# Kernel tuning notes

Measured on AMD Instinct MI355X. Metric: run time of the kernel, lower is better.

The kernel has to match this reference:

```python
import jax, jax.numpy as jnp
import numpy as np

N_HEADS = 16
HEAD_DIM = 64
HIDDEN = 1024


def setup_inputs() -> dict:
    key = jax.random.key(0)
    kx, kq, kk, kv, ko = jax.random.split(key, 5)
    B, S = 1, 4096
    # xavier_uniform for Linear(hidden, n_heads*head_dim): limit = sqrt(6/(fan_in+fan_out))
    lim = float(np.sqrt(6.0 / (HIDDEN + N_HEADS * HEAD_DIM)))
    x = jax.random.normal(kx, (B, S, HIDDEN), dtype=jnp.float32)
    wq = jax.random.uniform(kq, (N_HEADS * HEAD_DIM, HIDDEN), jnp.float32, -lim, lim)
    wk = jax.random.uniform(kk, (N_HEADS * HEAD_DIM, HIDDEN), jnp.float32, -lim, lim)
    wv = jax.random.uniform(kv, (N_HEADS * HEAD_DIM, HIDDEN), jnp.float32, -lim, lim)
    wo = jax.random.uniform(ko, (HIDDEN, N_HEADS * HEAD_DIM), jnp.float32, -lim, lim)
    return {"x": x, "wq": wq, "wk": wk, "wv": wv, "wo": wo}


def reference(x, wq, wk, wv, wo):
    B, S, _ = x.shape
    scale = HEAD_DIM ** -0.5
    # project and split heads: [B, H, S, D]
    def proj(w):
        return jnp.einsum('bsh,eh->bse', x, w).reshape(B, S, N_HEADS, HEAD_DIM).transpose(0, 2, 1, 3)
    q, k, v = proj(wq), proj(wk), proj(wv)
    scores = jnp.einsum('bhqd,bhkd->bhqk', q, k) * scale  # [B,H,S,S]
    causal = jnp.tril(jnp.ones((S, S), dtype=bool))
    scores = jnp.where(causal, scores, -jnp.inf)
    probs = jax.nn.softmax(scores, axis=-1)
    out = jnp.einsum('bhqk,bhkd->bhqd', probs, v)  # [B,H,S,D]
    out = out.transpose(0, 2, 1, 3).reshape(B, S, N_HEADS * HEAD_DIM)
    return jnp.einsum('bse,he->bsh', out, wo)
```

## Files before the change

### kernel.cpp

```cpp
#include <hip/hip_runtime.h>
#include <hip/hip_bf16.h>
#include <stdint.h>

typedef unsigned short u16;
typedef float f32x4 __attribute__((ext_vector_type(4)));
typedef __bf16 bf16x8 __attribute__((ext_vector_type(8)));
typedef u16 u16x8 __attribute__((ext_vector_type(8)));

#define GL2LDS16(g, l)                                                          \
  __builtin_amdgcn_global_load_lds(                                             \
      (const __attribute__((address_space(1))) unsigned int*)(g),               \
      (__attribute__((address_space(3))) unsigned int*)(l), 16, 0, 0)

#if __has_builtin(__builtin_amdgcn_exp2f)
#define EXP2(x) __builtin_amdgcn_exp2f(x)
#else
#define EXP2(x) exp2f(x)
#endif

#define SOFTMAX_SC 0.18033688f

__device__ __forceinline__ u16 f2bf(float f) {
  uint32_t u = __builtin_bit_cast(uint32_t, f);
  return (u16)((u + 0x7FFFu + ((u >> 16) & 1u)) >> 16);
}

__device__ __forceinline__ float bf2f(u16 b) {
  return __builtin_bit_cast(float, (uint32_t)b << 16);
}

__device__ __forceinline__ uint32_t cvt_pk_bf16(float lo, float hi) {
  uint32_t r;
  asm("v_cvt_pk_bf16_f32 %0, %1, %2" : "=v"(r) : "v"(lo), "v"(hi));
  return r;
}

__device__ __forceinline__ void cast8(const float* __restrict__ s,
                                      u16* __restrict__ d) {
  const float4* p = (const float4*)s;
  float4 a = p[0], b = p[1];
  uint4 o;
  o.x = cvt_pk_bf16(a.x, a.y);
  o.y = cvt_pk_bf16(a.z, a.w);
  o.z = cvt_pk_bf16(b.x, b.y);
  o.w = cvt_pk_bf16(b.z, b.w);
  *(uint4*)d = o;
}

__global__ __launch_bounds__(256) void cast_kernel(const float* __restrict__ s,
                                                   u16* __restrict__ d, int n) {
  int i = (blockIdx.x * 256 + threadIdx.x) * 8;
  if (i >= n) return;
  cast8(s + i, d + i);
}

__global__ __launch_bounds__(256) void cast4_kernel(const float* __restrict__ s0,
                                                    const float* __restrict__ s1,
                                                    const float* __restrict__ s2,
                                                    const float* __restrict__ s3,
                                                    u16* __restrict__ d) {
  int b = blockIdx.x >> 9;
  int i = ((blockIdx.x & 511) * 256 + threadIdx.x) * 8;
  const float* s = (b == 0) ? s0 : (b == 1) ? s1 : (b == 2) ? s2 : s3;
  cast8(s + i, d + ((size_t)b << 20) + i);
}

template <int MB>
__device__ __forceinline__ void mfma16(f32x4 (&acc)[8][4], const bf16x8 (&af)[4],
                                       const bf16x8 (&bfr)[4]) {
  asm volatile("s_waitcnt lgkmcnt(0)" ::: "memory");
  __builtin_amdgcn_sched_barrier(0);
  __builtin_amdgcn_s_setprio(1);
#pragma unroll
  for (int j = 0; j < 4; ++j)
#pragma unroll
    for (int n = 0; n < 4; ++n)
      acc[MB + j][n] = __builtin_amdgcn_mfma_f32_16x16x32_bf16(
          af[j], bfr[n], acc[MB + j][n], 0, 0, 0);
  __builtin_amdgcn_s_setprio(0);
}

__global__ __launch_bounds__(512, 2) void gemm8k(const u16* __restrict__ A,
                                                 const u16* __restrict__ B,
                                                 u16* __restrict__ C, int M,
                                                 int N, int K, int scaleq) {
  __shared__ u16 As[4][128 * 64];
  __shared__ u16 Bs[4][128 * 64];
  const int tid = threadIdx.x;
  const int lane = tid & 63;
  const int l15 = lane & 15, lhi = lane >> 4;
  const int wave = tid >> 6;
  const int wm = wave >> 2, wn = wave & 3;
  int bid = blockIdx.y * gridDim.x + blockIdx.x;
  const int cpx = (gridDim.x * gridDim.y) >> 3;
  bid = (bid & 7) * cpx + (bid >> 3);
  const int m0 = (bid / gridDim.x) * 256, n0 = (bid % gridDim.x) * 256;
  const int nt = K >> 6;

  int aoff[2][8], boff[2][4];
#pragma unroll
  for (int ks = 0; ks < 2; ++ks) {
    const int sl = ((ks * 4 + lhi) ^ (l15 & 7)) << 4;
#pragma unroll
    for (int m = 0; m < 8; ++m) aoff[ks][m] = (m * 16 + l15) * 128 + sl;
#pragma unroll
    for (int n = 0; n < 4; ++n)
      boff[ks][n] = ((wn & 1) * 64 + n * 16 + l15) * 128 + sl;
  }

  auto stA = [&](int T, int h) {
    u16* lb = As[(T & 1) * 2 + h];
#pragma unroll
    for (int i = 0; i < 2; ++i) {
      int c = tid + i * 512;
      int row = c >> 3;
      int scol = ((c & 7) ^ (row & 7)) * 8;
      GL2LDS16(A + (size_t)(m0 + h * 128 + row) * K + T * 64 + scol,
               (char*)lb + c * 16);
    }
  };
  auto stB = [&](int T, int h) {
    u16* lb = Bs[(T & 1) * 2 + h];
#pragma unroll
    for (int i = 0; i < 2; ++i) {
      int c = tid + i * 512;
      int row = c >> 3;
      int scol = ((c & 7) ^ (row & 7)) * 8;
      GL2LDS16(B + (size_t)(n0 + h * 128 + row) * K + T * 64 + scol,
               (char*)lb + c * 16);
    }
  };

  f32x4 acc[8][4] = {};

  stA(0, 0); stA(0, 1); stB(0, 0); stB(0, 1);
  asm volatile("s_waitcnt vmcnt(0)" ::: "memory");
  __builtin_amdgcn_s_barrier();

  for (int i = 0; i < nt / 2; ++i) {
    const int e = 2 * i, o = e + 1;
    const char* Ae = (const char*)As[wm];
    const char* Be = (const char*)Bs[wn >> 1];
    const char* Ao = (const char*)As[2 + wm];
    const char* Bo = (const char*)Bs[2 + (wn >> 1)];
    bf16x8 af[4], bfr[4];
    const bool pre = (e + 2) < nt;

    stA(o, 0); stA(o, 1);
    asm volatile("s_waitcnt vmcnt(4)" ::: "memory");
    __builtin_amdgcn_s_barrier();
#pragma unroll
    for (int j = 0; j < 4; ++j) af[j] = *(const bf16x8*)(Ae + aoff[0][j]);
#pragma unroll
    for (int n = 0; n < 4; ++n) bfr[n] = *(const bf16x8*)(Be + boff[0][n]);
    mfma16<0>(acc, af, bfr);
    __builtin_amdgcn_s_barrier();
#pragma unroll
    for (int j = 0; j < 4; ++j) af[j] = *(const bf16x8*)(Ae + aoff[0][4 + j]);
    stB(o, 0); stB(o, 1);
    __builtin_amdgcn_s_barrier();
    mfma16<4>(acc, af, bfr);
    __builtin_amdgcn_s_barrier();
#pragma unroll
    for (int j = 0; j < 4; ++j) af[j] = *(const bf16x8*)(Ae + aoff[1][j]);
#pragma unroll
    for (int n = 0; n < 4; ++n) bfr[n] = *(const bf16x8*)(Be + boff[1][n]);
    __builtin_amdgcn_s_barrier();
    mfma16<0>(acc, af, bfr);
    __builtin_amdgcn_s_barrier();
#pragma unroll
    for (int j = 0; j < 4; ++j) af[j] = *(const bf16x8*)(Ae + aoff[1][4 + j]);
    __builtin_amdgcn_s_barrier();
    mfma16<4>(acc, af, bfr);
    __builtin_amdgcn_s_barrier();
    if (pre) {
      stA(e + 2, 0); stA(e + 2, 1);
      asm volatile("s_waitcnt vmcnt(4)" ::: "memory");
    } else {
      asm volatile("s_waitcnt vmcnt(0)" ::: "memory");
    }
    __builtin_amdgcn_s_barrier();
#pragma unroll
    for (int j = 0; j < 4; ++j) af[j] = *(const bf16x8*)(Ao + aoff[0][j]);
#pragma unroll
    for (int n = 0; n < 4; ++n) bfr[n] = *(const bf16x8*)(Bo + boff[0][n]);
    mfma16<0>(acc, af, bfr);
    __builtin_amdgcn_s_barrier();
#pragma unroll
    for (int j = 0; j < 4; ++j) af[j] = *(const bf16x8*)(Ao + aoff[0][4 + j]);
    if (pre) { stB(e + 2, 0); stB(e + 2, 1); }
    __builtin_amdgcn_s_barrier();
    mfma16<4>(acc, af, bfr);
    __builtin_amdgcn_s_barrier();
#pragma unroll
    for (int j = 0; j < 4; ++j) af[j] = *(const bf16x8*)(Ao + aoff[1][j]);
#pragma unroll
    for (int n = 0; n < 4; ++n) bfr[n] = *(const bf16x8*)(Bo + boff[1][n]);
    __builtin_amdgcn_s_barrier();
    mfma16<0>(acc, af, bfr);
    __builtin_amdgcn_s_barrier();
#pragma unroll
    for (int j = 0; j < 4; ++j) af[j] = *(const bf16x8*)(Ao + aoff[1][4 + j]);
    __builtin_amdgcn_s_barrier();
    mfma16<4>(acc, af, bfr);
    __builtin_amdgcn_s_barrier();
  }

#pragma unroll
  for (int m = 0; m < 8; ++m) {
    int rbase = m0 + wm * 128 + m * 16 + lhi * 4;
#pragma unroll
    for (int n = 0; n < 4; ++n) {
      int col = n0 + wn * 64 + n * 16 + l15;
      float sc = (scaleq && col < 1024) ? SOFTMAX_SC : 1.0f;
#pragma unroll
      for (int r = 0; r < 4; ++r)
        C[(size_t)(rbase + r) * N + col] = f2bf(acc[m][n][r] * sc);
    }
  }
}

template <typename CT>
__global__ __launch_bounds__(256) void gemm_bt(const u16* __restrict__ A,
                                               const u16* __restrict__ B,
                                               CT* __restrict__ C, int M, int N,
                                               int K) {
  __shared__ u16 As[128 * 32];
  __shared__ u16 Bs[128 * 32];
  const int tid = threadIdx.x;
  const int lane = tid & 63;
  const int l15 = lane & 15, lhi = lane >> 4;
  const int wave = tid >> 6;
  const int wr = (wave >> 1) * 64, wc = (wave & 1) * 64;
  const int m0 = blockIdx.y * 128, n0 = blockIdx.x * 128;

  f32x4 acc[4][4] = {};

  for (int k0 = 0; k0 < K; k0 += 32) {
    __syncthreads();
#pragma unroll
    for (int i = 0; i < 2; ++i) {
      int c = tid + i * 256;
      int row = c >> 2, slot = c & 3;
      int scol = (slot ^ ((row >> 1) & 3)) * 8;
      GL2LDS16(A + (size_t)(m0 + row) * K + k0 + scol, (char*)As + c * 16);
      GL2LDS16(B + (size_t)(n0 + row) * K + k0 + scol, (char*)Bs + c * 16);
    }
    __syncthreads();
    bf16x8 af[4], bfr[4];
#pragma unroll
    for (int mi = 0; mi < 4; ++mi) {
      int row = wr + mi * 16 + l15;
      int byt = row * 64 + ((lhi ^ ((row >> 1) & 3)) << 4);
      af[mi] = *(const bf16x8*)((const char*)As + byt);
    }
#pragma unroll
    for (int ni = 0; ni < 4; ++ni) {
      int row = wc + ni * 16 + l15;
      int byt = row * 64 + ((lhi ^ ((row >> 1) & 3)) << 4);
      bfr[ni] = *(const bf16x8*)((const char*)Bs + byt);
    }
#pragma unroll
    for (int mi = 0; mi < 4; ++mi)
#pragma unroll
      for (int ni = 0; ni < 4; ++ni)
        acc[mi][ni] = __builtin_amdgcn_mfma_f32_16x16x32_bf16(
            af[mi], bfr[ni], acc[mi][ni], 0, 0, 0);
  }

#pragma unroll
  for (int mi = 0; mi < 4; ++mi) {
    int rbase = m0 + wr + mi * 16 + lhi * 4;
#pragma unroll
    for (int ni = 0; ni < 4; ++ni) {
      int col = n0 + wc + ni * 16 + l15;
#pragma unroll
      for (int r = 0; r < 4; ++r) {
        float v = acc[mi][ni][r];
        if constexpr (sizeof(CT) == 2)
          C[(size_t)(rbase + r) * N + col] = (CT)f2bf(v);
        else
          C[(size_t)(rbase + r) * N + col] = v;
      }
    }
  }
}

__global__ __launch_bounds__(256) void vtrans_kernel(const u16* __restrict__ qkv,
                                                     u16* __restrict__ vt) {
  __shared__ u16 t[64][72];
  const int bs = blockIdx.x * 64;
  const int be = blockIdx.y * 64;
  const int tid = threadIdx.x;
#pragma unroll
  for (int i = 0; i < 2; ++i) {
    int c = tid + i * 256, row = c >> 3, col = (c & 7) * 8;
    *(u16x8*)&t[row][col] =
        *(const u16x8*)(qkv + (size_t)(bs + row) * 3072 + 2048 + be + col);
  }
  __syncthreads();
#pragma unroll
  for (int i = 0; i < 2; ++i) {
    int c = tid + i * 256, erow = c >> 3, scol = (c & 7) * 8;
    u16x8 o;
#pragma unroll
    for (int j = 0; j < 8; ++j) o[j] = t[scol + j][erow];
    *(u16x8*)(vt + (size_t)(be + erow) * 4096 + bs + scol) = o;
  }
}

__global__ __launch_bounds__(512) void attn_kernel(const u16* __restrict__ qkv,
                                                   const u16* __restrict__ vt,
                                                   u16* __restrict__ pout,
                                                   float2* __restrict__ mlb) {
  const int h = blockIdx.y;
  const int bx = blockIdx.x;
  const int half = blockIdx.z;
  const int tid = threadIdx.x;
  const int lane = tid & 63, wave = tid >> 6;
  const int l15 = lane & 15, lhi = lane >> 4;

  u16* po = pout + (size_t)half * 4096 * 1024;
  float2* ml = mlb + (size_t)half * 4096 * 16;

  __shared__ u16 Ks[2][64 * 64];
  __shared__ u16 Vs[2][64 * 64];
  __shared__ u16 Ps[8][16 * 64];
  u16* Pw = Ps[wave];

  int koff[2][4];
#pragma unroll
  for (int ks = 0; ks < 2; ++ks)
#pragma unroll
    for (int nf = 0; nf < 4; ++nf) {
      int row = nf * 16 + l15;
      koff[ks][nf] = row * 128 + ((lhi * 16 + ks * 64) ^ ((row & 7) << 4));
    }
  int poff[4];
#pragma unroll
  for (int nf = 0; nf < 4; ++nf)
    poff[nf] = l15 * 128 + ((nf * 32 + lhi * 8) ^ ((l15 & 7) << 4));

  auto stage = [&](int b, int kb) {
    int c = tid;
    int row = c >> 3, slot = c & 7;
    int scol = (slot ^ (row & 7)) * 8;
    GL2LDS16(qkv + (size_t)(kb * 64 + row) * 3072 + 1024 + h * 64 + scol,
             (char*)(Ks[b]) + c * 16);
    GL2LDS16(vt + (size_t)(h * 64 + row) * 4096 + kb * 64 + scol,
             (char*)(Vs[b]) + c * 16);
  };

  int cur = 0;
  for (int rep = 0; rep < 2; ++rep) {
    const int qsb = rep ? (31 - bx) : bx;
    const int kb0 = half * (qsb + 1);
    const int kbe = kb0 + qsb + 1;
    const int q0 = qsb * 128 + wave * 16;
    const u16* Qb = qkv + (size_t)(q0 + l15) * 3072 + h * 64;
    bf16x8 qf0 = *(const bf16x8*)(const void*)(Qb + lhi * 8);
    bf16x8 qf1 = *(const bf16x8*)(const void*)(Qb + 32 + lhi * 8);

    f32x4 oa[4] = {};
    float mrow = -1e30f, lrow = 0.f;

    stage(cur, kb0);
    asm volatile("s_waitcnt vmcnt(0)" ::: "memory");
    __builtin_amdgcn_s_barrier();

    for (int kb = kb0; kb < kbe; ++kb) {
      if (kb + 1 < kbe) stage(cur ^ 1, kb + 1);

      f32x4 s[4] = {};
#pragma unroll
      for (int ks = 0; ks < 2; ++ks)
#pragma unroll
        for (int nf = 0; nf < 4; ++nf) {
          bf16x8 kf =
              *(const bf16x8*)((const char*)(Ks[cur]) + koff[ks][nf]);
          s[nf] = __builtin_amdgcn_mfma_f32_16x16x32_bf16(kf, ks ? qf1 : qf0,
                                                          s[nf], 0, 0, 0);
        }

      if (kb * 64 + 63 > q0) {
        const int q = q0 + l15;
#pragma unroll
        for (int nf = 0; nf < 4; ++nf)
#pragma unroll
          for (int r = 0; r < 4; ++r)
            if (kb * 64 + nf * 16 + lhi * 4 + r > q) s[nf][r] = -1e30f;
      }

      float pm0 = fmaxf(fmaxf(s[0][0], s[0][1]), fmaxf(s[0][2], s[0][3]));
      float pm1 = fmaxf(fmaxf(s[1][0], s[1][1]), fmaxf(s[1][2], s[1][3]));
      float pm2 = fmaxf(fmaxf(s[2][0], s[2][1]), fmaxf(s[2][2], s[2][3]));
      float pm3 = fmaxf(fmaxf(s[3][0], s[3][1]), fmaxf(s[3][2], s[3][3]));
      float pm = fmaxf(fmaxf(pm0, pm1), fmaxf(pm2, pm3));
      pm = fmaxf(pm, __shfl_xor(pm, 16));
      pm = fmaxf(pm, __shfl_xor(pm, 32));

      if (__any(pm - mrow > 8.0f)) {
        float mn = fmaxf(mrow, pm);
        float al = EXP2(mrow - mn);
        mrow = mn;
        lrow *= al;
        float alq[4];
#pragma unroll
        for (int r = 0; r < 4; ++r) alq[r] = __shfl(al, lhi * 4 + r, 16);
#pragma unroll
        for (int nf = 0; nf < 4; ++nf)
#pragma unroll
          for (int r = 0; r < 4; ++r) oa[nf][r] *= alq[r];
      }

#pragma unroll
      for (int nf = 0; nf < 4; ++nf)
#pragma unroll
        for (int r = 0; r < 4; ++r) s[nf][r] = EXP2(s[nf][r] - mrow);
      float rs = ((s[0][0] + s[0][1]) + (s[0][2] + s[0][3])) +
                 ((s[1][0] + s[1][1]) + (s[1][2] + s[1][3])) +
                 ((s[2][0] + s[2][1]) + (s[2][2] + s[2][3])) +
                 ((s[3][0] + s[3][1]) + (s[3][2] + s[3][3]));
      rs += __shfl_xor(rs, 16);
      rs += __shfl_xor(rs, 32);
      lrow += rs;

#pragma unroll
      for (int nf = 0; nf < 4; ++nf) {
        uint2 pk;
        pk.x = cvt_pk_bf16(s[nf][0], s[nf][1]);
        pk.y = cvt_pk_bf16(s[nf][2], s[nf][3]);
        *(uint2*)((char*)Pw + poff[nf]) = pk;
      }

      bf16x8 pf[2];
#pragma unroll
      for (int ks = 0; ks < 2; ++ks)
        pf[ks] = *(const bf16x8*)((const char*)Pw + koff[ks][0]);

#pragma unroll
      for (int ks = 0; ks < 2; ++ks)
#pragma unroll
        for (int nf = 0; nf < 4; ++nf) {
          bf16x8 vf =
              *(const bf16x8*)((const char*)(Vs[cur]) + koff[ks][nf]);
          oa[nf] = __builtin_amdgcn_mfma_f32_16x16x32_bf16(pf[ks], vf, oa[nf],
                                                           0, 0, 0);
        }

      asm volatile("s_waitcnt vmcnt(0)" ::: "memory");
      __builtin_amdgcn_s_barrier();
      cur ^= 1;
    }

    float linv[4];
#pragma unroll
    for (int r = 0; r < 4; ++r)
      linv[r] = 1.0f / __shfl(lrow, lhi * 4 + r, 16);
#pragma unroll
    for (int r = 0; r < 4; ++r) {
      int rowg = q0 + lhi * 4 + r;
#pragma unroll
      for (int nf = 0; nf < 4; ++nf)
        po[(size_t)rowg * 1024 + h * 64 + nf * 16 + l15] =
            f2bf(oa[nf][r] * linv[r]);
    }
    if (lhi == 0) ml[(q0 + l15) * 16 + h] = float2{mrow, lrow};
  }
}

__global__ __launch_bounds__(256) void merge_kernel(const u16* __restrict__ po,
                                                    const float2* __restrict__ mlb,
                                                    u16* __restrict__ atn) {
  int base = (blockIdx.x * 256 + threadIdx.x) * 8;
  int row = base >> 10, h = (base & 1023) >> 6;
  float2 a = mlb[row * 16 + h];
  float2 b = mlb[4096 * 16 + row * 16 + h];
  float m = fmaxf(a.x, b.x);
  float w0 = EXP2(a.x - m) * a.y, w1 = EXP2(b.x - m) * b.y;
  float inv = 1.0f / (w0 + w1);
  w0 *= inv; w1 *= inv;
  u16x8 p0 = *(const u16x8*)(po + base);
  u16x8 p1 = *(const u16x8*)(po + 4096 * 1024 + base);
  u16x8 o;
#pragma unroll
  for (int j = 0; j < 8; ++j) o[j] = f2bf(w0 * bf2f(p0[j]) + w1 * bf2f(p1[j]));
  *(u16x8*)(atn + base) = o;
}

extern "C" void kernel_launch(void* const* d_in, const int* in_sizes, int n_in,
                              void* d_out, int out_size, void* d_ws,
                              size_t ws_size, hipStream_t stream) {
  const float* x = (const float*)d_in[0];
  const float* wq = (const float*)d_in[1];
  const float* wk = (const float*)d_in[2];
  const float* wv = (const float*)d_in[3];
  const float* wo = (const float*)d_in[4];

  u16* xb = (u16*)d_ws;
  u16* wqkv = xb + 4096 * 1024;
  u16* wob = wqkv + 3072 * 1024;
  u16* qkv = wob + 1024 * 1024;
  u16* atn = qkv + (size_t)4096 * 3072;
  u16* vt = xb;
  float2* mlb = (float2*)wqkv;
  u16* pout = (u16*)d_out;

  cast_kernel<<<2048, 256, 0, stream>>>(x, xb, 4096 * 1024);
  cast4_kernel<<<2048, 256, 0, stream>>>(wq, wk, wv, wo, wqkv);

  gemm8k<<<dim3(12, 16), 512, 0, stream>>>(xb, wqkv, qkv, 4096, 3072, 1024, 1);
  vtrans_kernel<<<dim3(64, 16), 256, 0, stream>>>(qkv, vt);
  attn_kernel<<<dim3(16, 16, 2), 512, 0, stream>>>(qkv, vt, pout, mlb);
  merge_kernel<<<2048, 256, 0, stream>>>(pout, mlb, atn);
  gemm_bt<float><<<dim3(8, 32), 256, 0, stream>>>(atn, wob, (float*)d_out, 4096,
                                                  1024, 1024);
}
```

Measured before the change: 219.9 us.

## Fuse casts, write split Q/K/transposed V from QKV GEMM, 3-way attention split, pipelined out-proj

Merges the two cast kernels into one launch. The QKV GEMM epilogue now writes Q, K and an already transposed V into separate buffers, which removes the separate V-transpose kernel. Attention splits the key range three ways instead of two, adding empty-split handling, and the merge kernel combines three partials in place. The output projection gets a double-buffered 64-wide K tile pipeline using async global-to-LDS loads. The costs are an extra partial buffer to merge and strided 8-byte stores for V^T in the GEMM epilogue.

```diff
diff --git a/kernel.cpp b/kernel.cpp
--- a/kernel.cpp
+++ b/kernel.cpp
@@ -47,22 +47,22 @@
   *(uint4*)d = o;
 }
 
-__global__ __launch_bounds__(256) void cast_kernel(const float* __restrict__ s,
-                                                   u16* __restrict__ d, int n) {
-  int i = (blockIdx.x * 256 + threadIdx.x) * 8;
-  if (i >= n) return;
-  cast8(s + i, d + i);
-}
-
-__global__ __launch_bounds__(256) void cast4_kernel(const float* __restrict__ s0,
-                                                    const float* __restrict__ s1,
-                                                    const float* __restrict__ s2,
-                                                    const float* __restrict__ s3,
-                                                    u16* __restrict__ d) {
-  int b = blockIdx.x >> 9;
-  int i = ((blockIdx.x & 511) * 256 + threadIdx.x) * 8;
-  const float* s = (b == 0) ? s0 : (b == 1) ? s1 : (b == 2) ? s2 : s3;
-  cast8(s + i, d + ((size_t)b << 20) + i);
+__global__ __launch_bounds__(256) void castall_kernel(
+    const float* __restrict__ x, const float* __restrict__ wq,
+    const float* __restrict__ wk, const float* __restrict__ wv,
+    const float* __restrict__ wo, u16* __restrict__ xb,
+    u16* __restrict__ wqkv) {
+  int b = blockIdx.x;
+  if (b < 2048) {
+    int i = (b * 256 + threadIdx.x) * 8;
+    cast8(x + i, xb + i);
+  } else {
+    b -= 2048;
+    int w = b >> 9;
+    int i = ((b & 511) * 256 + threadIdx.x) * 8;
+    const float* s = (w == 0) ? wq : (w == 1) ? wk : (w == 2) ? wv : wo;
+    cast8(s + i, wqkv + ((size_t)w << 20) + i);
+  }
 }
 
 template <int MB>
@@ -82,8 +82,10 @@
 
 __global__ __launch_bounds__(512, 2) void gemm8k(const u16* __restrict__ A,
                                                  const u16* __restrict__ B,
-                                                 u16* __restrict__ C, int M,
-                                                 int N, int K, int scaleq) {
+                                                 u16* __restrict__ qb,
+                                                 u16* __restrict__ kb,
+                                                 u16* __restrict__ vt) {
+  const int K = 1024;
   __shared__ u16 As[4][128 * 64];
   __shared__ u16 Bs[4][128 * 64];
   const int tid = threadIdx.x;
@@ -212,60 +214,92 @@
 #pragma unroll
     for (int n = 0; n < 4; ++n) {
       int col = n0 + wn * 64 + n * 16 + l15;
-      float sc = (scaleq && col < 1024) ? SOFTMAX_SC : 1.0f;
-#pragma unroll
-      for (int r = 0; r < 4; ++r)
-        C[(size_t)(rbase + r) * N + col] = f2bf(acc[m][n][r] * sc);
-    }
-  }
-}
-
-template <typename CT>
-__global__ __launch_bounds__(256) void gemm_bt(const u16* __restrict__ A,
-                                               const u16* __restrict__ B,
-                                               CT* __restrict__ C, int M, int N,
-                                               int K) {
-  __shared__ u16 As[128 * 32];
-  __shared__ u16 Bs[128 * 32];
+      if (col >= 2048) {
+        uint2 pk;
+        pk.x = cvt_pk_bf16(acc[m][n][0], acc[m][n][1]);
+        pk.y = cvt_pk_bf16(acc[m][n][2], acc[m][n][3]);
+        *(uint2*)(vt + (size_t)(col - 2048) * 4096 + rbase) = pk;
+      } else {
+        u16* dst = (col < 1024) ? qb : kb;
+        int cc = col & 1023;
+        float sc = (col < 1024) ? SOFTMAX_SC : 1.0f;
+#pragma unroll
+        for (int r = 0; r < 4; ++r)
+          dst[(size_t)(rbase + r) * 1024 + cc] = f2bf(acc[m][n][r] * sc);
+      }
+    }
+  }
+}
+
+__global__ __launch_bounds__(256) void gemm2p(const u16* __restrict__ A,
+                                              const u16* __restrict__ B,
+                                              float* __restrict__ C, int M,
+                                              int N, int K) {
+  __shared__ u16 As[2][128 * 64];
+  __shared__ u16 Bs[2][128 * 64];
   const int tid = threadIdx.x;
   const int lane = tid & 63;
   const int l15 = lane & 15, lhi = lane >> 4;
   const int wave = tid >> 6;
   const int wr = (wave >> 1) * 64, wc = (wave & 1) * 64;
   const int m0 = blockIdx.y * 128, n0 = blockIdx.x * 128;
+  const int nt = K >> 6;
+
+  int aoff[2][4], boff[2][4];
+#pragma unroll
+  for (int ks = 0; ks < 2; ++ks) {
+    const int sl = ((ks * 4 + lhi) ^ (l15 & 7)) << 4;
+#pragma unroll
+    for (int mi = 0; mi < 4; ++mi)
+      aoff[ks][mi] = (wr + mi * 16 + l15) * 128 + sl;
+#pragma unroll
+    for (int ni = 0; ni < 4; ++ni)
+      boff[ks][ni] = (wc + ni * 16 + l15) * 128 + sl;
+  }
+
+  auto stage = [&](int b, int t) {
+#pragma unroll
+    for (int i = 0; i < 4; ++i) {
+      int c = tid + i * 256;
+      int row = c >> 3;
+      int scol = ((c & 7) ^ (row & 7)) * 8;
+      GL2LDS16(A + (size_t)(m0 + row) * K + t * 64 + scol,
+               (char*)(As[b]) + c * 16);
+      GL2LDS16(B + (size_t)(n0 + row) * K + t * 64 + scol,
+               (char*)(Bs[b]) + c * 16);
+    }
+  };
 
   f32x4 acc[4][4] = {};
 
-  for (int k0 = 0; k0 < K; k0 += 32) {
-    __syncthreads();
-#pragma unroll
-    for (int i = 0; i < 2; ++i) {
-      int c = tid + i * 256;
-      int row = c >> 2, slot = c & 3;
-      int scol = (slot ^ ((row >> 1) & 3)) * 8;
-      GL2LDS16(A + (size_t)(m0 + row) * K + k0 + scol, (char*)As + c * 16);
-      GL2LDS16(B + (size_t)(n0 + row) * K + k0 + scol, (char*)Bs + c * 16);
-    }
-    __syncthreads();
-    bf16x8 af[4], bfr[4];
-#pragma unroll
-    for (int mi = 0; mi < 4; ++mi) {
-      int row = wr + mi * 16 + l15;
-      int byt = row * 64 + ((lhi ^ ((row >> 1) & 3)) << 4);
-      af[mi] = *(const bf16x8*)((const char*)As + byt);
-    }
-#pragma unroll
-    for (int ni = 0; ni < 4; ++ni) {
-      int row = wc + ni * 16 + l15;
-      int byt = row * 64 + ((lhi ^ ((row >> 1) & 3)) << 4);
-      bfr[ni] = *(const bf16x8*)((const char*)Bs + byt);
-    }
-#pragma unroll
-    for (int mi = 0; mi < 4; ++mi)
+  stage(0, 0);
+  asm volatile("s_waitcnt vmcnt(0)" ::: "memory");
+  __builtin_amdgcn_s_barrier();
+
+  int cur = 0;
+  for (int t = 0; t < nt; ++t) {
+    if (t + 1 < nt) stage(cur ^ 1, t + 1);
+    const char* Ab = (const char*)(As[cur]);
+    const char* Bb = (const char*)(Bs[cur]);
+#pragma unroll
+    for (int ks = 0; ks < 2; ++ks) {
+      bf16x8 af[4], bfr[4];
+#pragma unroll
+      for (int mi = 0; mi < 4; ++mi)
+        af[mi] = *(const bf16x8*)(Ab + aoff[ks][mi]);
 #pragma unroll
       for (int ni = 0; ni < 4; ++ni)
-        acc[mi][ni] = __builtin_amdgcn_mfma_f32_16x16x32_bf16(
-            af[mi], bfr[ni], acc[mi][ni], 0, 0, 0);
+        bfr[ni] = *(const bf16x8*)(Bb + boff[ks][ni]);
+#pragma unroll
+      for (int mi = 0; mi < 4; ++mi)
+#pragma unroll
+        for (int ni = 0; ni < 4; ++ni)
+          acc[mi][ni] = __builtin_amdgcn_mfma_f32_16x16x32_bf16(
+              af[mi], bfr[ni], acc[mi][ni], 0, 0, 0);
+    }
+    asm volatile("s_waitcnt vmcnt(0)" ::: "memory");
+    __builtin_amdgcn_s_barrier();
+    cur ^= 1;
   }
 
 #pragma unroll
@@ -275,53 +309,25 @@
     for (int ni = 0; ni < 4; ++ni) {
       int col = n0 + wc + ni * 16 + l15;
 #pragma unroll
-      for (int r = 0; r < 4; ++r) {
-        float v = acc[mi][ni][r];
-        if constexpr (sizeof(CT) == 2)
-          C[(size_t)(rbase + r) * N + col] = (CT)f2bf(v);
-        else
-          C[(size_t)(rbase + r) * N + col] = v;
-      }
-    }
-  }
-}
-
-__global__ __launch_bounds__(256) void vtrans_kernel(const u16* __restrict__ qkv,
-                                                     u16* __restrict__ vt) {
-  __shared__ u16 t[64][72];
-  const int bs = blockIdx.x * 64;
-  const int be = blockIdx.y * 64;
-  const int tid = threadIdx.x;
-#pragma unroll
-  for (int i = 0; i < 2; ++i) {
-    int c = tid + i * 256, row = c >> 3, col = (c & 7) * 8;
-    *(u16x8*)&t[row][col] =
-        *(const u16x8*)(qkv + (size_t)(bs + row) * 3072 + 2048 + be + col);
-  }
-  __syncthreads();
-#pragma unroll
-  for (int i = 0; i < 2; ++i) {
-    int c = tid + i * 256, erow = c >> 3, scol = (c & 7) * 8;
-    u16x8 o;
-#pragma unroll
-    for (int j = 0; j < 8; ++j) o[j] = t[scol + j][erow];
-    *(u16x8*)(vt + (size_t)(be + erow) * 4096 + bs + scol) = o;
-  }
-}
-
-__global__ __launch_bounds__(512) void attn_kernel(const u16* __restrict__ qkv,
-                                                   const u16* __restrict__ vt,
-                                                   u16* __restrict__ pout,
-                                                   float2* __restrict__ mlb) {
+      for (int r = 0; r < 4; ++r)
+        C[(size_t)(rbase + r) * N + col] = acc[mi][ni][r];
+    }
+  }
+}
+
+__global__ __launch_bounds__(512) void attn_kernel(
+    const u16* __restrict__ qb, const u16* __restrict__ kbuf,
+    const u16* __restrict__ vt, u16* __restrict__ p0, u16* __restrict__ p12,
+    float2* __restrict__ mlb) {
   const int h = blockIdx.y;
   const int bx = blockIdx.x;
-  const int half = blockIdx.z;
+  const int z = blockIdx.z;
   const int tid = threadIdx.x;
   const int lane = tid & 63, wave = tid >> 6;
   const int l15 = lane & 15, lhi = lane >> 4;
 
-  u16* po = pout + (size_t)half * 4096 * 1024;
-  float2* ml = mlb + (size_t)half * 4096 * 16;
+  u16* po = (z == 0) ? p0 : p12 + (size_t)(z - 1) * 4096 * 1024;
+  float2* ml = mlb + (size_t)z * 4096 * 16;
 
   __shared__ u16 Ks[2][64 * 64];
   __shared__ u16 Vs[2][64 * 64];
@@ -345,7 +351,7 @@
     int c = tid;
     int row = c >> 3, slot = c & 7;
     int scol = (slot ^ (row & 7)) * 8;
-    GL2LDS16(qkv + (size_t)(kb * 64 + row) * 3072 + 1024 + h * 64 + scol,
+    GL2LDS16(kbuf + (size_t)(kb * 64 + row) * 1024 + h * 64 + scol,
              (char*)(Ks[b]) + c * 16);
     GL2LDS16(vt + (size_t)(h * 64 + row) * 4096 + kb * 64 + scol,
              (char*)(Vs[b]) + c * 16);
@@ -354,10 +360,17 @@
   int cur = 0;
   for (int rep = 0; rep < 2; ++rep) {
     const int qsb = rep ? (31 - bx) : bx;
-    const int kb0 = half * (qsb + 1);
-    const int kbe = kb0 + qsb + 1;
+    const int T = 2 * qsb + 2;
+    const int kb0 = (z * T) / 3;
+    const int kbe = ((z + 1) * T) / 3;
     const int q0 = qsb * 128 + wave * 16;
-    const u16* Qb = qkv + (size_t)(q0 + l15) * 3072 + h * 64;
+
+    if (kb0 >= kbe) {
+      if (lhi == 0) ml[(q0 + l15) * 16 + h] = float2{-1e30f, 0.f};
+      continue;
+    }
+
+    const u16* Qb = qb + (size_t)(q0 + l15) * 1024 + h * 64;
     bf16x8 qf0 = *(const bf16x8*)(const void*)(Qb + lhi * 8);
     bf16x8 qf1 = *(const bf16x8*)(const void*)(Qb + 32 + lhi * 8);
 
@@ -376,8 +389,7 @@
       for (int ks = 0; ks < 2; ++ks)
 #pragma unroll
         for (int nf = 0; nf < 4; ++nf) {
-          bf16x8 kf =
-              *(const bf16x8*)((const char*)(Ks[cur]) + koff[ks][nf]);
+          bf16x8 kf = *(const bf16x8*)((const char*)(Ks[cur]) + koff[ks][nf]);
           s[nf] = __builtin_amdgcn_mfma_f32_16x16x32_bf16(kf, ks ? qf1 : qf0,
                                                           s[nf], 0, 0, 0);
         }
@@ -442,8 +454,7 @@
       for (int ks = 0; ks < 2; ++ks)
 #pragma unroll
         for (int nf = 0; nf < 4; ++nf) {
-          bf16x8 vf =
-              *(const bf16x8*)((const char*)(Vs[cur]) + koff[ks][nf]);
+          bf16x8 vf = *(const bf16x8*)((const char*)(Vs[cur]) + koff[ks][nf]);
           oa[nf] = __builtin_amdgcn_mfma_f32_16x16x32_bf16(pf[ks], vf, oa[nf],
                                                            0, 0, 0);
         }
@@ -455,8 +466,10 @@
 
     float linv[4];
 #pragma unroll
-    for (int r = 0; r < 4; ++r)
-      linv[r] = 1.0f / __shfl(lrow, lhi * 4 + r, 16);
+    for (int r = 0; r < 4; ++r) {
+      float lr = __shfl(lrow, lhi * 4 + r, 16);
+      linv[r] = (lr > 0.f) ? 1.0f / lr : 0.f;
+    }
 #pragma unroll
     for (int r = 0; r < 4; ++r) {
       int rowg = q0 + lhi * 4 + r;
@@ -469,23 +482,29 @@
   }
 }
 
-__global__ __launch_bounds__(256) void merge_kernel(const u16* __restrict__ po,
+__global__ __launch_bounds__(256) void merge_kernel(u16* __restrict__ p0,
+                                                    const u16* __restrict__ p12,
                                                     const float2* __restrict__ mlb,
-                                                    u16* __restrict__ atn) {
+                                                    int dummy) {
   int base = (blockIdx.x * 256 + threadIdx.x) * 8;
   int row = base >> 10, h = (base & 1023) >> 6;
   float2 a = mlb[row * 16 + h];
   float2 b = mlb[4096 * 16 + row * 16 + h];
-  float m = fmaxf(a.x, b.x);
-  float w0 = EXP2(a.x - m) * a.y, w1 = EXP2(b.x - m) * b.y;
-  float inv = 1.0f / (w0 + w1);
-  w0 *= inv; w1 *= inv;
-  u16x8 p0 = *(const u16x8*)(po + base);
-  u16x8 p1 = *(const u16x8*)(po + 4096 * 1024 + base);
+  float2 c = mlb[2 * 4096 * 16 + row * 16 + h];
+  float m = fmaxf(fmaxf(a.x, b.x), c.x);
+  float w0 = EXP2(a.x - m) * a.y;
+  float w1 = EXP2(b.x - m) * b.y;
+  float w2 = EXP2(c.x - m) * c.y;
+  float inv = 1.0f / (w0 + w1 + w2);
+  w0 *= inv; w1 *= inv; w2 *= inv;
+  u16x8 q0 = *(const u16x8*)(p0 + base);
+  u16x8 q1 = *(const u16x8*)(p12 + base);
+  u16x8 q2 = *(const u16x8*)(p12 + 4096 * 1024 + base);
   u16x8 o;
 #pragma unroll
-  for (int j = 0; j < 8; ++j) o[j] = f2bf(w0 * bf2f(p0[j]) + w1 * bf2f(p1[j]));
-  *(u16x8*)(atn + base) = o;
+  for (int j = 0; j < 8; ++j)
+    o[j] = f2bf(w0 * bf2f(q0[j]) + w1 * bf2f(q1[j]) + w2 * bf2f(q2[j]));
+  *(u16x8*)(p0 + base) = o;
 }
 
 extern "C" void kernel_launch(void* const* d_in, const int* in_sizes, int n_in,
@@ -500,19 +519,18 @@
   u16* xb = (u16*)d_ws;
   u16* wqkv = xb + 4096 * 1024;
   u16* wob = wqkv + 3072 * 1024;
-  u16* qkv = wob + 1024 * 1024;
-  u16* atn = qkv + (size_t)4096 * 3072;
-  u16* vt = xb;
+  u16* qb = wob + 1024 * 1024;
+  u16* kbuf = qb + 4096 * 1024;
+  u16* vt = kbuf + 4096 * 1024;
+  u16* atn = vt + 4096 * 1024;
   float2* mlb = (float2*)wqkv;
-  u16* pout = (u16*)d_out;
-
-  cast_kernel<<<2048, 256, 0, stream>>>(x, xb, 4096 * 1024);
-  cast4_kernel<<<2048, 256, 0, stream>>>(wq, wk, wv, wo, wqkv);
-
-  gemm8k<<<dim3(12, 16), 512, 0, stream>>>(xb, wqkv, qkv, 4096, 3072, 1024, 1);
-  vtrans_kernel<<<dim3(64, 16), 256, 0, stream>>>(qkv, vt);
-  attn_kernel<<<dim3(16, 16, 2), 512, 0, stream>>>(qkv, vt, pout, mlb);
-  merge_kernel<<<2048, 256, 0, stream>>>(pout, mlb, atn);
-  gemm_bt<float><<<dim3(8, 32), 256, 0, stream>>>(atn, wob, (float*)d_out, 4096,
-                                                  1024, 1024);
-}
+  u16* p12 = (u16*)d_out;
+
+  castall_kernel<<<4096, 256, 0, stream>>>(x, wq, wk, wv, wo, xb, wqkv);
+
+  gemm8k<<<dim3(12, 16), 512, 0, stream>>>(xb, wqkv, qb, kbuf, vt);
+  attn_kernel<<<dim3(16, 16, 3), 512, 0, stream>>>(qb, kbuf, vt, atn, p12, mlb);
+  merge_kernel<<<2048, 256, 0, stream>>>(atn, p12, mlb, 0);
+  gemm2p<<<dim3(8, 32), 256, 0, stream>>>(atn, wob, (float*)d_out, 4096, 1024,
+                                          1024);
+}
```

Result: no change. 216.6 us (-1.5%).
